# Performance work log

Measured on AMD Instinct MI355X. Metric: run time of the kernel, lower is better.

Reference implementation:

```python
import jax, jax.numpy as jnp
import numpy as np

NUM_BINS = 512  # 8 levels per RGB channel: (R>>5)<<6 + (G>>5)<<3 + (B>>5)


def _color_histograms(frames):
    # frames: [B, T, H, W, 3] int32, values in [0, 256)
    B, T, H, W, _ = frames.shape
    f = frames.reshape(B * T, H * W, 3)
    R, G, Bc = f[:, :, 0], f[:, :, 1], f[:, :, 2]
    binned = ((R >> 5) << 6) + ((G >> 5) << 3) + (Bc >> 5)  # [BT, HW] in [0,512)
    prefix = (jnp.arange(B * T, dtype=jnp.int32) << 9)[:, None]  # frame offset (512 bins/frame)
    idx = (binned + prefix).reshape(-1)
    hist = jnp.zeros(B * T * NUM_BINS, dtype=jnp.int32).at[idx].add(jnp.int32(1))
    hist = hist.reshape(B, T, NUM_BINS).astype(jnp.float32)
    # F.normalize(p=2, dim=2, eps=1e-12)
    norm = jnp.sqrt(jnp.sum(hist * hist, axis=2, keepdims=True))
    return hist / jnp.maximum(norm, 1e-12)


def setup_inputs() -> dict:
    key = jax.random.key(0)
    k1, k2, k3 = jax.random.split(key, 3)
    frames = jax.random.randint(k1, (16, 256, 64, 64, 3), 0, 256, dtype=jnp.int32)
    fc_w = jax.random.normal(k2, (128, 101), dtype=jnp.float32) * 0.1
    fc_b = jax.random.normal(k3, (128,), dtype=jnp.float32) * 0.01
    return {"frames": frames, "fc_w": fc_w, "fc_b": fc_b}


def reference(frames, fc_w, fc_b):
    lookup_window = fc_w.shape[1]
    half = (lookup_window - 1) // 2
    x = _color_histograms(frames)  # [B, T, 512]
    B, T, _ = x.shape
    sim = jnp.einsum('btd,bsd->bts', x, x)  # [B, T, T]
    sim_padded = jnp.pad(sim, ((0, 0), (0, 0), (half, half)))  # [B, T, T+W-1]
    t_idx = jnp.arange(T)[:, None]                    # [T, 1]
    l_idx = t_idx + jnp.arange(lookup_window)[None, :]  # [T, W]
    windowed = sim_padded[:, t_idx, l_idx]            # [B, T, W]
    return jax.nn.relu(jnp.einsum('btw,ow->bto', windowed, fc_w) + fc_b)
```

## Files before the change

### kernel.cpp

```cpp
#include <hip/hip_runtime.h>
#include <hip/hip_bf16.h>

#define NUM_BINS 512
#define T_LEN 256
#define B_LEN 16
#define WIN 101
#define HALF 50
#define NOUT 128

typedef __attribute__((ext_vector_type(8))) short short8;
typedef __attribute__((ext_vector_type(4))) float f32x4;

__device__ __forceinline__ unsigned short f2bf(float f) {
    unsigned u = __float_as_uint(f);
    u += 0x7fff + ((u >> 16) & 1);
    return (unsigned short)(u >> 16);
}

__global__ __launch_bounds__(256) void hist_kernel(const int* __restrict__ frames,
                                                   __hip_bfloat16* __restrict__ xout) {
    __shared__ int hist[NUM_BINS];
    __shared__ float red[4];
    const int f = blockIdx.x;
    const int tid = threadIdx.x;

    hist[tid] = 0;
    hist[tid + 256] = 0;
    __syncthreads();

    const int4* base = (const int4*)(frames + (size_t)f * 12288);
    #pragma unroll
    for (int g = 0; g < 4; ++g) {
        int4 a = base[tid * 12 + g * 3 + 0];
        int4 b = base[tid * 12 + g * 3 + 1];
        int4 c = base[tid * 12 + g * 3 + 2];
        atomicAdd(&hist[((a.x >> 5) << 6) | ((a.y >> 5) << 3) | (a.z >> 5)], 1);
        atomicAdd(&hist[((a.w >> 5) << 6) | ((b.x >> 5) << 3) | (b.y >> 5)], 1);
        atomicAdd(&hist[((b.z >> 5) << 6) | ((b.w >> 5) << 3) | (c.x >> 5)], 1);
        atomicAdd(&hist[((c.y >> 5) << 6) | ((c.z >> 5) << 3) | (c.w >> 5)], 1);
    }
    __syncthreads();

    const int h0 = hist[tid];
    const int h1 = hist[tid + 256];
    float ss = (float)h0 * (float)h0 + (float)h1 * (float)h1;
    #pragma unroll
    for (int off = 32; off; off >>= 1) ss += __shfl_down(ss, off, 64);
    const int lane = tid & 63;
    const int wave = tid >> 6;
    if (lane == 0) red[wave] = ss;
    __syncthreads();
    const float tot = red[0] + red[1] + red[2] + red[3];
    const float inv = 1.0f / sqrtf(tot);
    __hip_bfloat16* xrow = xout + (size_t)f * NUM_BINS;
    xrow[tid] = __float2bfloat16((float)h0 * inv);
    xrow[tid + 256] = __float2bfloat16((float)h1 * inv);
}

__global__ __launch_bounds__(256) void simfc_kernel(const unsigned short* __restrict__ x,
                                                    const float* __restrict__ fc_w,
                                                    const float* __restrict__ fc_b,
                                                    float* __restrict__ out) {
    __shared__ float sim_lds[16 * 132];
    __shared__ unsigned short win_lds[16 * 136];

    const int bid = blockIdx.x;
    const int b = bid & 15;
    const int tt = bid >> 4;
    const int t0 = tt * 16;
    const int tid = threadIdx.x;
    const int lane = tid & 63;
    const int wave = tid >> 6;
    const int l15 = lane & 15;
    const int kg = lane >> 4;

    const unsigned short* xb = x + (size_t)b * T_LEN * NUM_BINS;

    f32x4 acc0 = {0.f, 0.f, 0.f, 0.f};
    f32x4 acc1 = {0.f, 0.f, 0.f, 0.f};
    const short8 zero8 = {0, 0, 0, 0, 0, 0, 0, 0};
    {
        const int rowA = t0 + l15;
        const int s0 = t0 - HALF + 32 * wave;
        const int rb0 = s0 + l15;
        const int rb1 = s0 + 16 + l15;
        const bool v0 = (rb0 >= 0) && (rb0 < T_LEN);
        const bool v1 = (rb1 >= 0) && (rb1 < T_LEN);
        const int rc0 = min(max(rb0, 0), T_LEN - 1);
        const int rc1 = min(max(rb1, 0), T_LEN - 1);
        const unsigned short* pa = xb + (size_t)rowA * NUM_BINS + kg * 8;
        const unsigned short* p0 = xb + (size_t)rc0 * NUM_BINS + kg * 8;
        const unsigned short* p1 = xb + (size_t)rc1 * NUM_BINS + kg * 8;
        #pragma unroll
        for (int ks = 0; ks < 16; ++ks) {
            short8 a  = *(const short8*)(pa + ks * 32);
            short8 b0 = *(const short8*)(p0 + ks * 32);
            short8 b1 = *(const short8*)(p1 + ks * 32);
            b0 = v0 ? b0 : zero8;
            b1 = v1 ? b1 : zero8;
            acc0 = __builtin_amdgcn_mfma_f32_16x16x32_bf16(a, b0, acc0, 0, 0, 0);
            acc1 = __builtin_amdgcn_mfma_f32_16x16x32_bf16(a, b1, acc1, 0, 0, 0);
        }
        const int j0 = 2 * wave;
        #pragma unroll
        for (int r = 0; r < 4; ++r) {
            const int row = kg * 4 + r;
            sim_lds[row * 132 + j0 * 16 + l15] = acc0[r];
            sim_lds[row * 132 + (j0 + 1) * 16 + l15] = acc1[r];
        }
    }
    __syncthreads();

    {
        const int i = tid >> 4;
        const int w8 = (tid & 15) * 8;
        short8 v;
        #pragma unroll
        for (int e = 0; e < 8; ++e) {
            const int w = w8 + e;
            const float f = (w < WIN) ? sim_lds[i * 132 + i + w] : 0.0f;
            v[e] = (short)f2bf(f);
        }
        *(short8*)(&win_lds[i * 136 + w8]) = v;
    }
    __syncthreads();

    {
        f32x4 o0 = {0.f, 0.f, 0.f, 0.f};
        f32x4 o1 = {0.f, 0.f, 0.f, 0.f};
        const int n0 = wave * 32;
        const int oA = n0 + l15;
        const int oB = n0 + 16 + l15;
        const float* pwA = fc_w + oA * WIN;
        const float* pwB = fc_w + oB * WIN;
        #pragma unroll
        for (int ks = 0; ks < 4; ++ks) {
            const int wbase = ks * 32 + kg * 8;
            short8 a = *(const short8*)(&win_lds[l15 * 136 + wbase]);
            short8 b0, b1;
            #pragma unroll
            for (int e = 0; e < 8; ++e) {
                const int w = wbase + e;
                const int wc = min(w, WIN - 1);
                float vA = pwA[wc];
                float vB = pwB[wc];
                b0[e] = (short)((w < WIN) ? f2bf(vA) : (unsigned short)0);
                b1[e] = (short)((w < WIN) ? f2bf(vB) : (unsigned short)0);
            }
            o0 = __builtin_amdgcn_mfma_f32_16x16x32_bf16(a, b0, o0, 0, 0, 0);
            o1 = __builtin_amdgcn_mfma_f32_16x16x32_bf16(a, b1, o1, 0, 0, 0);
        }
        const float biasA = fc_b[oA];
        const float biasB = fc_b[oB];
        float* ob = out + ((size_t)b * T_LEN + t0) * NOUT;
        #pragma unroll
        for (int r = 0; r < 4; ++r) {
            const int row = kg * 4 + r;
            ob[row * NOUT + oA] = fmaxf(o0[r] + biasA, 0.0f);
            ob[row * NOUT + oB] = fmaxf(o1[r] + biasB, 0.0f);
        }
    }
}

extern "C" void kernel_launch(void* const* d_in, const int* in_sizes, int n_in,
                              void* d_out, int out_size, void* d_ws, size_t ws_size,
                              hipStream_t stream) {
    const int* frames = (const int*)d_in[0];
    const float* fc_w = (const float*)d_in[1];
    const float* fc_b = (const float*)d_in[2];
    float* out = (float*)d_out;
    __hip_bfloat16* x = (__hip_bfloat16*)d_ws;

    hist_kernel<<<B_LEN * T_LEN, 256, 0, stream>>>(frames, x);
    simfc_kernel<<<B_LEN * T_LEN / 16, 256, 0, stream>>>((const unsigned short*)x, fc_w, fc_b, out);
}
```

Baseline: 53.69 us.

## Coalesce pixel loads in histogram and double waves per sim/fc block

```diff
diff --git a/kernel.cpp b/kernel.cpp
--- a/kernel.cpp
+++ b/kernel.cpp
@@ -28,16 +28,12 @@
     hist[tid + 256] = 0;
     __syncthreads();
 
-    const int4* base = (const int4*)(frames + (size_t)f * 12288);
-    #pragma unroll
-    for (int g = 0; g < 4; ++g) {
-        int4 a = base[tid * 12 + g * 3 + 0];
-        int4 b = base[tid * 12 + g * 3 + 1];
-        int4 c = base[tid * 12 + g * 3 + 2];
-        atomicAdd(&hist[((a.x >> 5) << 6) | ((a.y >> 5) << 3) | (a.z >> 5)], 1);
-        atomicAdd(&hist[((a.w >> 5) << 6) | ((b.x >> 5) << 3) | (b.y >> 5)], 1);
-        atomicAdd(&hist[((b.z >> 5) << 6) | ((b.w >> 5) << 3) | (c.x >> 5)], 1);
-        atomicAdd(&hist[((c.y >> 5) << 6) | ((c.z >> 5) << 3) | (c.w >> 5)], 1);
+    const int* base = frames + (size_t)f * 12288;
+    #pragma unroll 4
+    for (int i = 0; i < 16; ++i) {
+        const int p = i * 256 + tid;
+        int3 v = *(const int3*)(base + (size_t)p * 3);
+        atomicAdd(&hist[((v.x >> 5) << 6) | ((v.y >> 5) << 3) | (v.z >> 5)], 1);
     }
     __syncthreads();
 
@@ -57,7 +53,7 @@
     xrow[tid + 256] = __float2bfloat16((float)h1 * inv);
 }
 
-__global__ __launch_bounds__(256) void simfc_kernel(const unsigned short* __restrict__ x,
+__global__ __launch_bounds__(512) void simfc_kernel(const unsigned short* __restrict__ x,
                                                     const float* __restrict__ fc_w,
                                                     const float* __restrict__ fc_b,
                                                     float* __restrict__ out) {
@@ -76,50 +72,37 @@
 
     const unsigned short* xb = x + (size_t)b * T_LEN * NUM_BINS;
 
-    f32x4 acc0 = {0.f, 0.f, 0.f, 0.f};
-    f32x4 acc1 = {0.f, 0.f, 0.f, 0.f};
-    const short8 zero8 = {0, 0, 0, 0, 0, 0, 0, 0};
     {
+        f32x4 acc = {0.f, 0.f, 0.f, 0.f};
+        const short8 zero8 = {0, 0, 0, 0, 0, 0, 0, 0};
         const int rowA = t0 + l15;
-        const int s0 = t0 - HALF + 32 * wave;
-        const int rb0 = s0 + l15;
-        const int rb1 = s0 + 16 + l15;
-        const bool v0 = (rb0 >= 0) && (rb0 < T_LEN);
-        const bool v1 = (rb1 >= 0) && (rb1 < T_LEN);
-        const int rc0 = min(max(rb0, 0), T_LEN - 1);
-        const int rc1 = min(max(rb1, 0), T_LEN - 1);
+        const int rb = t0 - HALF + 16 * wave + l15;
+        const bool vv = (rb >= 0) && (rb < T_LEN);
+        const int rc = min(max(rb, 0), T_LEN - 1);
         const unsigned short* pa = xb + (size_t)rowA * NUM_BINS + kg * 8;
-        const unsigned short* p0 = xb + (size_t)rc0 * NUM_BINS + kg * 8;
-        const unsigned short* p1 = xb + (size_t)rc1 * NUM_BINS + kg * 8;
+        const unsigned short* ps = xb + (size_t)rc * NUM_BINS + kg * 8;
         #pragma unroll
         for (int ks = 0; ks < 16; ++ks) {
             short8 a  = *(const short8*)(pa + ks * 32);
-            short8 b0 = *(const short8*)(p0 + ks * 32);
-            short8 b1 = *(const short8*)(p1 + ks * 32);
-            b0 = v0 ? b0 : zero8;
-            b1 = v1 ? b1 : zero8;
-            acc0 = __builtin_amdgcn_mfma_f32_16x16x32_bf16(a, b0, acc0, 0, 0, 0);
-            acc1 = __builtin_amdgcn_mfma_f32_16x16x32_bf16(a, b1, acc1, 0, 0, 0);
+            short8 bb = *(const short8*)(ps + ks * 32);
+            bb = vv ? bb : zero8;
+            acc = __builtin_amdgcn_mfma_f32_16x16x32_bf16(a, bb, acc, 0, 0, 0);
         }
-        const int j0 = 2 * wave;
         #pragma unroll
-        for (int r = 0; r < 4; ++r) {
-            const int row = kg * 4 + r;
-            sim_lds[row * 132 + j0 * 16 + l15] = acc0[r];
-            sim_lds[row * 132 + (j0 + 1) * 16 + l15] = acc1[r];
-        }
+        for (int r = 0; r < 4; ++r)
+            sim_lds[(kg * 4 + r) * 132 + wave * 16 + l15] = acc[r];
     }
     __syncthreads();
 
-    {
+    if (tid < 256) {
         const int i = tid >> 4;
         const int w8 = (tid & 15) * 8;
         short8 v;
         #pragma unroll
         for (int e = 0; e < 8; ++e) {
             const int w = w8 + e;
-            const float f = (w < WIN) ? sim_lds[i * 132 + i + w] : 0.0f;
-            v[e] = (short)f2bf(f);
+            const float fv = (w < WIN) ? sim_lds[i * 132 + i + w] : 0.0f;
+            v[e] = (short)f2bf(fv);
         }
         *(short8*)(&win_lds[i * 136 + w8]) = v;
     }
@@ -127,38 +110,25 @@
 
     {
         f32x4 o0 = {0.f, 0.f, 0.f, 0.f};
-        f32x4 o1 = {0.f, 0.f, 0.f, 0.f};
-        const int n0 = wave * 32;
-        const int oA = n0 + l15;
-        const int oB = n0 + 16 + l15;
-        const float* pwA = fc_w + oA * WIN;
-        const float* pwB = fc_w + oB * WIN;
+        const int o = wave * 16 + l15;
+        const float* pw = fc_w + o * WIN;
         #pragma unroll
         for (int ks = 0; ks < 4; ++ks) {
             const int wbase = ks * 32 + kg * 8;
             short8 a = *(const short8*)(&win_lds[l15 * 136 + wbase]);
-            short8 b0, b1;
+            short8 b0;
             #pragma unroll
             for (int e = 0; e < 8; ++e) {
                 const int w = wbase + e;
-                const int wc = min(w, WIN - 1);
-                float vA = pwA[wc];
-                float vB = pwB[wc];
-                b0[e] = (short)((w < WIN) ? f2bf(vA) : (unsigned short)0);
-                b1[e] = (short)((w < WIN) ? f2bf(vB) : (unsigned short)0);
+                b0[e] = (short)((w < WIN) ? f2bf(pw[w]) : (unsigned short)0);
             }
             o0 = __builtin_amdgcn_mfma_f32_16x16x32_bf16(a, b0, o0, 0, 0, 0);
-            o1 = __builtin_amdgcn_mfma_f32_16x16x32_bf16(a, b1, o1, 0, 0, 0);
         }
-        const float biasA = fc_b[oA];
-        const float biasB = fc_b[oB];
+        const float bias = fc_b[o];
         float* ob = out + ((size_t)b * T_LEN + t0) * NOUT;
         #pragma unroll
-        for (int r = 0; r < 4; ++r) {
-            const int row = kg * 4 + r;
-            ob[row * NOUT + oA] = fmaxf(o0[r] + biasA, 0.0f);
-            ob[row * NOUT + oB] = fmaxf(o1[r] + biasB, 0.0f);
-        }
+        for (int r = 0; r < 4; ++r)
+            ob[(kg * 4 + r) * NOUT + o] = fmaxf(o0[r] + bias, 0.0f);
     }
 }
 
@@ -172,5 +142,5 @@
     __hip_bfloat16* x = (__hip_bfloat16*)d_ws;
 
     hist_kernel<<<B_LEN * T_LEN, 256, 0, stream>>>(frames, x);
-    simfc_kernel<<<B_LEN * T_LEN / 16, 256, 0, stream>>>((const unsigned short*)x, fc_w, fc_b, out);
+    simfc_kernel<<<B_LEN * T_LEN / 16, 512, 0, stream>>>((const unsigned short*)x, fc_w, fc_b, out);
 }
```

New measurement: 44.86 us. -16.5%, faster.
